# Kernel optimization log

Hardware: AMD Instinct MI355X
Metric: run time of the kernel (lower is better)

## Reference

```python
import jax, jax.numpy as jnp
import numpy as np

TAU = 2.0
V_TH = 1.0


def setup_inputs() -> dict:
    key = jax.random.key(0)
    k1, k2, k3 = jax.random.split(key, 3)
    T, B, H = 128, 64, 1024
    x = jax.random.normal(k1, (T, B, H), dtype=jnp.float32)
    # nn.Linear(H, H, bias=False) weights, shape [out, in]
    W1 = jax.random.normal(k2, (H, H), dtype=jnp.float32) / np.sqrt(H)
    W2 = jax.random.normal(k3, (H, H), dtype=jnp.float32) / np.sqrt(H)
    return {"x": x, "W1": W1, "W2": W2}


def _lif_scan(x_proj):
    # x_proj: [T, B, H]; membrane v starts at 0.
    def step(v, xt):
        h = v + (xt - v) / TAU          # leaky integrate
        s = (h >= V_TH).astype(h.dtype)  # hard-threshold spike
        v_new = h * (1.0 - s)            # soft reset (to 0 on spike)
        return v_new, s

    v0 = jnp.zeros(x_proj.shape[1:], dtype=x_proj.dtype)
    _, spikes = jax.lax.scan(step, v0, x_proj)
    return spikes  # [T, B, H]


def reference(x, W1, W2):
    # fc1 applied per timestep == one batched GEMM over [T*B, H]
    x_proj = jnp.einsum('tbh,oh->tbo', x, W1)
    spike = _lif_scan(x_proj)
    out = jnp.einsum('tbh,oh->tbo', spike, W2)
    return out
```

## Files before the change

### kernel.cpp

```cpp
#include <hip/hip_runtime.h>
#include <hip/hip_bf16.h>
#include <stdint.h>

#define TT 128
#define BB 64
#define HH 1024
#define MM (TT * BB)
#define NLANE (BB * HH)
#define DELTA 3.0e-4
#define CAPL 32768

typedef __attribute__((ext_vector_type(8))) short bf16x8;
typedef __attribute__((ext_vector_type(4))) float f32x4;

#define GLOAD16(g, l)                                                        \
    __builtin_amdgcn_global_load_lds(                                        \
        (const __attribute__((address_space(1))) unsigned int*)(g),          \
        (__attribute__((address_space(3))) unsigned int*)(l), 16, 0, 0)

static __device__ __forceinline__ unsigned short bf16_bits(float f) {
    __hip_bfloat16 b = __float2bfloat16(f);
    return *reinterpret_cast<unsigned short*>(&b);
}

__global__ __launch_bounds__(256) void split2_kernel(const float* __restrict__ src,
                                                     unsigned short* __restrict__ hi,
                                                     unsigned short* __restrict__ lo,
                                                     int n4) {
    const int i = blockIdx.x * 256 + threadIdx.x;
    if (i >= n4) return;
    float4 x = reinterpret_cast<const float4*>(src)[i];
    float v[4] = {x.x, x.y, x.z, x.w};
    unsigned short hb[4], lb[4];
#pragma unroll
    for (int c = 0; c < 4; c++) {
        hb[c] = bf16_bits(v[c]);
        __hip_bfloat16 hh = *reinterpret_cast<__hip_bfloat16*>(&hb[c]);
        lb[c] = bf16_bits(v[c] - __bfloat162float(hh));
    }
    reinterpret_cast<ushort4*>(hi)[i] = make_ushort4(hb[0], hb[1], hb[2], hb[3]);
    reinterpret_cast<ushort4*>(lo)[i] = make_ushort4(lb[0], lb[1], lb[2], lb[3]);
}

__global__ __launch_bounds__(256) void cast_bf16(const float* __restrict__ src,
                                                 unsigned short* __restrict__ dst,
                                                 int n) {
    const int i = blockIdx.x * 256 + threadIdx.x;
    if (i < n) dst[i] = bf16_bits(src[i]);
}

__global__ __launch_bounds__(256) void gemm1_mfma(const unsigned short* __restrict__ Ah,
                                                  const unsigned short* __restrict__ Al,
                                                  const unsigned short* __restrict__ Bh,
                                                  const unsigned short* __restrict__ Bl,
                                                  float* __restrict__ C) {
    __shared__ short AsH[128 * 32];
    __shared__ short AsL[128 * 32];
    __shared__ short BsH[128 * 32];
    __shared__ short BsL[128 * 32];

    const int tid = threadIdx.x;
    const int lane = tid & 63;
    const int wave = tid >> 6;
    const int m0 = blockIdx.x * 128;
    const int n0 = blockIdx.y * 128;
    const int wm = (wave >> 1) * 64;
    const int wn = (wave & 1) * 64;

    const int rsel = lane & 15;
    const int qk = (lane >> 4) * 8;

    f32x4 acc[4][4] = {};

    for (int k0 = 0; k0 < HH; k0 += 32) {
#pragma unroll
        for (int p = 0; p < 2; p++) {
            const int c = tid + p * 256;
            const int cb = wave * 64 + p * 256;
            const int row = c >> 2;
            const int part = c & 3;
            const size_t goA = (size_t)(m0 + row) * HH + k0 + part * 8;
            const size_t goB = (size_t)(n0 + row) * HH + k0 + part * 8;
            GLOAD16(&Ah[goA], &AsH[cb * 8]);
            GLOAD16(&Al[goA], &AsL[cb * 8]);
            GLOAD16(&Bh[goB], &BsH[cb * 8]);
            GLOAD16(&Bl[goB], &BsL[cb * 8]);
        }
        __syncthreads();

        bf16x8 aH[4], aL[4], bH[4], bL[4];
#pragma unroll
        for (int mi = 0; mi < 4; mi++) {
            const int r = (wm + mi * 16 + rsel) * 32 + qk;
            aH[mi] = *reinterpret_cast<bf16x8*>(&AsH[r]);
            aL[mi] = *reinterpret_cast<bf16x8*>(&AsL[r]);
        }
#pragma unroll
        for (int ni = 0; ni < 4; ni++) {
            const int r = (wn + ni * 16 + rsel) * 32 + qk;
            bH[ni] = *reinterpret_cast<bf16x8*>(&BsH[r]);
            bL[ni] = *reinterpret_cast<bf16x8*>(&BsL[r]);
        }

#pragma unroll
        for (int mi = 0; mi < 4; mi++)
#pragma unroll
            for (int ni = 0; ni < 4; ni++) {
                acc[mi][ni] = __builtin_amdgcn_mfma_f32_16x16x32_bf16(aH[mi], bH[ni], acc[mi][ni], 0, 0, 0);
                acc[mi][ni] = __builtin_amdgcn_mfma_f32_16x16x32_bf16(aH[mi], bL[ni], acc[mi][ni], 0, 0, 0);
                acc[mi][ni] = __builtin_amdgcn_mfma_f32_16x16x32_bf16(aL[mi], bH[ni], acc[mi][ni], 0, 0, 0);
            }

        __syncthreads();
    }

    const int col = lane & 15;
    const int quad = lane >> 4;
#pragma unroll
    for (int mi = 0; mi < 4; mi++)
#pragma unroll
        for (int ni = 0; ni < 4; ni++) {
            const int m = m0 + wm + mi * 16 + quad * 4;
            const int n = n0 + wn + ni * 16 + col;
            float* dst = &C[(size_t)m * HH + n];
#pragma unroll
            for (int r = 0; r < 4; r++)
                dst[(size_t)r * HH] = acc[mi][ni][r];
        }
}

__global__ __launch_bounds__(256) void lif_scan_flag(const float* __restrict__ xp,
                                                     unsigned short* __restrict__ sp,
                                                     int* __restrict__ count,
                                                     int* __restrict__ list) {
    const int idx = blockIdx.x * 256 + threadIdx.x;
    double v = 0.0;
    bool flg = false;
#pragma unroll 4
    for (int t = 0; t < TT; t++) {
        const double x = (double)xp[(size_t)t * NLANE + idx];
        const double h = v + (x - v) * 0.5;
        const bool s = (h >= 1.0);
        flg |= (fabs(h - 1.0) < DELTA);
        v = s ? 0.0 : h;
        sp[(size_t)t * NLANE + idx] = s ? (unsigned short)0x3F80 : (unsigned short)0;
    }
    if (flg) {
        const int i = atomicAdd(count, 1);
        list[i] = idx;
    }
}

__global__ __launch_bounds__(256) void recompute_dots(const float* __restrict__ X,
                                                      const float* __restrict__ W1,
                                                      const int* __restrict__ count,
                                                      const int* __restrict__ list,
                                                      double* __restrict__ hraw) {
    const int cnt = *count;
    const int lim = (cnt < CAPL ? cnt : CAPL);
    const long ntask = (long)lim * TT;
    const int ln = threadIdx.x & 63;
    const long wid = (long)blockIdx.x * 4 + (threadIdx.x >> 6);
    const long nwaves = (long)gridDim.x * 4;

    for (long task = wid; task < ntask; task += nwaves) {
        const int li = (int)(task >> 7);
        const int t = (int)(task & (TT - 1));
        const int lane = list[li];
        const int b = lane >> 10;
        const int h = lane & (HH - 1);
        const float4* x4 = reinterpret_cast<const float4*>(X + (size_t)(t * BB + b) * HH);
        const float4* w4 = reinterpret_cast<const float4*>(W1 + (size_t)h * HH);

        double s0 = 0.0, s1 = 0.0, s2 = 0.0, s3 = 0.0;
#pragma unroll
        for (int i = 0; i < 4; i++) {
            const float4 xa = x4[ln + i * 64];
            const float4 wa = w4[ln + i * 64];
            s0 = fma((double)xa.x, (double)wa.x, s0);
            s1 = fma((double)xa.y, (double)wa.y, s1);
            s2 = fma((double)xa.z, (double)wa.z, s2);
            s3 = fma((double)xa.w, (double)wa.w, s3);
        }
        double s = (s0 + s1) + (s2 + s3);
#pragma unroll
        for (int off = 32; off >= 1; off >>= 1)
            s += __shfl_down(s, off);
        if (ln == 0) hraw[task] = s;
    }
}

__global__ __launch_bounds__(256) void rescan_lanes(const float* __restrict__ X,
                                                    const float* __restrict__ W1,
                                                    const int* __restrict__ count,
                                                    const int* __restrict__ list,
                                                    const double* __restrict__ hraw,
                                                    unsigned short* __restrict__ sp) {
    const int li = blockIdx.x * 256 + threadIdx.x;
    const int cnt = *count;
    if (li >= cnt) return;
    const int lane = list[li];

    double v = 0.0;
    if (li < CAPL) {
        const double* hb = hraw + (size_t)li * TT;
        for (int t = 0; t < TT; t++) {
            const double h = v + (hb[t] - v) * 0.5;
            const bool s = (h >= 1.0);
            v = s ? 0.0 : h;
            sp[(size_t)t * NLANE + lane] = s ? (unsigned short)0x3F80 : (unsigned short)0;
        }
    } else {
        const int b = lane >> 10;
        const int h = lane & (HH - 1);
        const float* wrow = W1 + (size_t)h * HH;
        for (int t = 0; t < TT; t++) {
            const float* xrow = X + (size_t)(t * BB + b) * HH;
            double d = 0.0;
            for (int k = 0; k < HH; k++)
                d = fma((double)xrow[k], (double)wrow[k], d);
            const double hh = v + (d - v) * 0.5;
            const bool s = (hh >= 1.0);
            v = s ? 0.0 : hh;
            sp[(size_t)t * NLANE + lane] = s ? (unsigned short)0x3F80 : (unsigned short)0;
        }
    }
}

__global__ __launch_bounds__(256) void gemm2_mfma(const unsigned short* __restrict__ S,
                                                  const unsigned short* __restrict__ W,
                                                  float* __restrict__ O) {
    __shared__ short As[128 * 32];
    __shared__ short Bs[128 * 32];

    const int tid = threadIdx.x;
    const int lane = tid & 63;
    const int wave = tid >> 6;
    const int m0 = blockIdx.x * 128;
    const int n0 = blockIdx.y * 128;
    const int wm = (wave >> 1) * 64;
    const int wn = (wave & 1) * 64;

    const int rsel = lane & 15;
    const int qk = (lane >> 4) * 8;

    f32x4 acc[4][4] = {};

    for (int k0 = 0; k0 < HH; k0 += 32) {
#pragma unroll
        for (int p = 0; p < 2; p++) {
            const int c = tid + p * 256;
            const int cb = wave * 64 + p * 256;
            const int row = c >> 2;
            const int part = c & 3;
            GLOAD16(&S[(size_t)(m0 + row) * HH + k0 + part * 8], &As[cb * 8]);
            GLOAD16(&W[(size_t)(n0 + row) * HH + k0 + part * 8], &Bs[cb * 8]);
        }
        __syncthreads();

        bf16x8 a[4], b[4];
#pragma unroll
        for (int mi = 0; mi < 4; mi++)
            a[mi] = *reinterpret_cast<bf16x8*>(&As[(wm + mi * 16 + rsel) * 32 + qk]);
#pragma unroll
        for (int ni = 0; ni < 4; ni++)
            b[ni] = *reinterpret_cast<bf16x8*>(&Bs[(wn + ni * 16 + rsel) * 32 + qk]);

#pragma unroll
        for (int mi = 0; mi < 4; mi++)
#pragma unroll
            for (int ni = 0; ni < 4; ni++)
                acc[mi][ni] = __builtin_amdgcn_mfma_f32_16x16x32_bf16(
                    a[mi], b[ni], acc[mi][ni], 0, 0, 0);

        __syncthreads();
    }

    const int col = lane & 15;
    const int quad = lane >> 4;
#pragma unroll
    for (int mi = 0; mi < 4; mi++)
#pragma unroll
        for (int ni = 0; ni < 4; ni++) {
            const int m = m0 + wm + mi * 16 + quad * 4;
            const int n = n0 + wn + ni * 16 + col;
            float* dst = &O[(size_t)m * HH + n];
#pragma unroll
            for (int r = 0; r < 4; r++)
                dst[(size_t)r * HH] = acc[mi][ni][r];
        }
}

extern "C" void kernel_launch(void* const* d_in, const int* in_sizes, int n_in,
                              void* d_out, int out_size, void* d_ws, size_t ws_size,
                              hipStream_t stream) {
    const float* x  = (const float*)d_in[0];
    const float* W1 = (const float*)d_in[1];
    const float* W2 = (const float*)d_in[2];
    float* out = (float*)d_out;

    char* ws = (char*)d_ws;
    const size_t szX = (size_t)MM * HH;
    const size_t szW = (size_t)HH * HH;

    unsigned short* Xhi  = (unsigned short*)ws;
    unsigned short* Xlo  = Xhi + szX;
    unsigned short* W1hi = Xlo + szX;
    unsigned short* W1lo = W1hi + szW;
    unsigned short* w2b  = W1lo + szW;
    int*            list = (int*)(w2b + szW);
    int*            cnt  = list + NLANE;
    float*          xp   = (float*)(((uintptr_t)(cnt + 64) + 255) & ~(uintptr_t)255);
    unsigned short* sp   = Xhi;
    double*         hraw = (double*)xp;

    hipMemsetAsync(cnt, 0, sizeof(int), stream);

    split2_kernel<<<(int)(szX / 4 / 256), 256, 0, stream>>>(x, Xhi, Xlo, (int)(szX / 4));
    split2_kernel<<<(int)(szW / 4 / 256), 256, 0, stream>>>(W1, W1hi, W1lo, (int)(szW / 4));
    cast_bf16<<<(int)((szW + 255) / 256), 256, 0, stream>>>(W2, w2b, (int)szW);

    dim3 g1(MM / 128, HH / 128);
    gemm1_mfma<<<g1, 256, 0, stream>>>(Xhi, Xlo, W1hi, W1lo, xp);

    lif_scan_flag<<<NLANE / 256, 256, 0, stream>>>(xp, sp, cnt, list);

    recompute_dots<<<2048, 256, 0, stream>>>(x, W1, cnt, list, hraw);
    rescan_lanes<<<NLANE / 256, 256, 0, stream>>>(x, W1, cnt, list, hraw, sp);

    dim3 g2(MM / 128, HH / 128);
    gemm2_mfma<<<g2, 256, 0, stream>>>(sp, w2b, out);
}
```

Measured before the change: 258.9 us.

## Switch split GEMMs to fp16 with scaled low part, swizzle LDS, tighten flag band

Replaces the bf16 hi/lo split with an fp16 split whose low residual is scaled by 4096. The cross terms go into a separate accumulator and are recombined at the end. The higher precision lets the near-threshold flag band shrink tenfold, so fewer lanes go through the exact fp64 recompute and rescan path. It also adds an XOR swizzle to the LDS layout in both GEMMs to reduce bank conflicts, at the cost of a second accumulator set (more registers) and fp16 range risk on inputs.

```diff
diff --git a/kernel.cpp b/kernel.cpp
--- a/kernel.cpp
+++ b/kernel.cpp
@@ -7,10 +7,12 @@
 #define HH 1024
 #define MM (TT * BB)
 #define NLANE (BB * HH)
-#define DELTA 3.0e-4
+#define DELTA 3.0e-5
 #define CAPL 32768
-
-typedef __attribute__((ext_vector_type(8))) short bf16x8;
+#define LO_SCALE 4096.0f
+#define F16_ONE 0x3C00
+
+typedef __attribute__((ext_vector_type(8))) _Float16 f16x8;
 typedef __attribute__((ext_vector_type(4))) float f32x4;
 
 #define GLOAD16(g, l)                                                        \
@@ -18,9 +20,9 @@
         (const __attribute__((address_space(1))) unsigned int*)(g),          \
         (__attribute__((address_space(3))) unsigned int*)(l), 16, 0, 0)
 
-static __device__ __forceinline__ unsigned short bf16_bits(float f) {
-    __hip_bfloat16 b = __float2bfloat16(f);
-    return *reinterpret_cast<unsigned short*>(&b);
+static __device__ __forceinline__ unsigned short f16_bits(float f) {
+    _Float16 h = (_Float16)f;
+    return *reinterpret_cast<unsigned short*>(&h);
 }
 
 __global__ __launch_bounds__(256) void split2_kernel(const float* __restrict__ src,
@@ -34,19 +36,19 @@
     unsigned short hb[4], lb[4];
 #pragma unroll
     for (int c = 0; c < 4; c++) {
-        hb[c] = bf16_bits(v[c]);
-        __hip_bfloat16 hh = *reinterpret_cast<__hip_bfloat16*>(&hb[c]);
-        lb[c] = bf16_bits(v[c] - __bfloat162float(hh));
+        _Float16 hh = (_Float16)v[c];
+        hb[c] = *reinterpret_cast<unsigned short*>(&hh);
+        lb[c] = f16_bits((v[c] - (float)hh) * LO_SCALE);
     }
     reinterpret_cast<ushort4*>(hi)[i] = make_ushort4(hb[0], hb[1], hb[2], hb[3]);
     reinterpret_cast<ushort4*>(lo)[i] = make_ushort4(lb[0], lb[1], lb[2], lb[3]);
 }
 
-__global__ __launch_bounds__(256) void cast_bf16(const float* __restrict__ src,
-                                                 unsigned short* __restrict__ dst,
-                                                 int n) {
+__global__ __launch_bounds__(256) void cast_f16(const float* __restrict__ src,
+                                                unsigned short* __restrict__ dst,
+                                                int n) {
     const int i = blockIdx.x * 256 + threadIdx.x;
-    if (i < n) dst[i] = bf16_bits(src[i]);
+    if (i < n) dst[i] = f16_bits(src[i]);
 }
 
 __global__ __launch_bounds__(256) void gemm1_mfma(const unsigned short* __restrict__ Ah,
@@ -68,9 +70,19 @@
     const int wn = (wave & 1) * 64;
 
     const int rsel = lane & 15;
-    const int qk = (lane >> 4) * 8;
-
-    f32x4 acc[4][4] = {};
+    const int part = lane >> 4;
+
+    int adrA[4], adrB[4];
+#pragma unroll
+    for (int i = 0; i < 4; i++) {
+        const int ra = wm + i * 16 + rsel;
+        const int rb = wn + i * 16 + rsel;
+        adrA[i] = ra * 32 + (part ^ ((ra >> 1) & 3)) * 8;
+        adrB[i] = rb * 32 + (part ^ ((rb >> 1) & 3)) * 8;
+    }
+
+    f32x4 acc1[4][4] = {};
+    f32x4 acc2[4][4] = {};
 
     for (int k0 = 0; k0 < HH; k0 += 32) {
 #pragma unroll
@@ -78,9 +90,10 @@
             const int c = tid + p * 256;
             const int cb = wave * 64 + p * 256;
             const int row = c >> 2;
-            const int part = c & 3;
-            const size_t goA = (size_t)(m0 + row) * HH + k0 + part * 8;
-            const size_t goB = (size_t)(n0 + row) * HH + k0 + part * 8;
+            const int pslot = c & 3;
+            const int pdata = pslot ^ ((row >> 1) & 3);
+            const size_t goA = (size_t)(m0 + row) * HH + k0 + pdata * 8;
+            const size_t goB = (size_t)(n0 + row) * HH + k0 + pdata * 8;
             GLOAD16(&Ah[goA], &AsH[cb * 8]);
             GLOAD16(&Al[goA], &AsL[cb * 8]);
             GLOAD16(&Bh[goB], &BsH[cb * 8]);
@@ -88,27 +101,25 @@
         }
         __syncthreads();
 
-        bf16x8 aH[4], aL[4], bH[4], bL[4];
+        f16x8 aH[4], aL[4], bH[4], bL[4];
 #pragma unroll
         for (int mi = 0; mi < 4; mi++) {
-            const int r = (wm + mi * 16 + rsel) * 32 + qk;
-            aH[mi] = *reinterpret_cast<bf16x8*>(&AsH[r]);
-            aL[mi] = *reinterpret_cast<bf16x8*>(&AsL[r]);
+            aH[mi] = *reinterpret_cast<f16x8*>(&AsH[adrA[mi]]);
+            aL[mi] = *reinterpret_cast<f16x8*>(&AsL[adrA[mi]]);
         }
 #pragma unroll
         for (int ni = 0; ni < 4; ni++) {
-            const int r = (wn + ni * 16 + rsel) * 32 + qk;
-            bH[ni] = *reinterpret_cast<bf16x8*>(&BsH[r]);
-            bL[ni] = *reinterpret_cast<bf16x8*>(&BsL[r]);
+            bH[ni] = *reinterpret_cast<f16x8*>(&BsH[adrB[ni]]);
+            bL[ni] = *reinterpret_cast<f16x8*>(&BsL[adrB[ni]]);
         }
 
 #pragma unroll
         for (int mi = 0; mi < 4; mi++)
 #pragma unroll
             for (int ni = 0; ni < 4; ni++) {
-                acc[mi][ni] = __builtin_amdgcn_mfma_f32_16x16x32_bf16(aH[mi], bH[ni], acc[mi][ni], 0, 0, 0);
-                acc[mi][ni] = __builtin_amdgcn_mfma_f32_16x16x32_bf16(aH[mi], bL[ni], acc[mi][ni], 0, 0, 0);
-                acc[mi][ni] = __builtin_amdgcn_mfma_f32_16x16x32_bf16(aL[mi], bH[ni], acc[mi][ni], 0, 0, 0);
+                acc1[mi][ni] = __builtin_amdgcn_mfma_f32_16x16x32_f16(aH[mi], bH[ni], acc1[mi][ni], 0, 0, 0);
+                acc2[mi][ni] = __builtin_amdgcn_mfma_f32_16x16x32_f16(aH[mi], bL[ni], acc2[mi][ni], 0, 0, 0);
+                acc2[mi][ni] = __builtin_amdgcn_mfma_f32_16x16x32_f16(aL[mi], bH[ni], acc2[mi][ni], 0, 0, 0);
             }
 
         __syncthreads();
@@ -116,6 +127,7 @@
 
     const int col = lane & 15;
     const int quad = lane >> 4;
+    const float inv = 1.0f / LO_SCALE;
 #pragma unroll
     for (int mi = 0; mi < 4; mi++)
 #pragma unroll
@@ -125,7 +137,7 @@
             float* dst = &C[(size_t)m * HH + n];
 #pragma unroll
             for (int r = 0; r < 4; r++)
-                dst[(size_t)r * HH] = acc[mi][ni][r];
+                dst[(size_t)r * HH] = fmaf(acc2[mi][ni][r], inv, acc1[mi][ni][r]);
         }
 }
 
@@ -143,7 +155,7 @@
         const bool s = (h >= 1.0);
         flg |= (fabs(h - 1.0) < DELTA);
         v = s ? 0.0 : h;
-        sp[(size_t)t * NLANE + idx] = s ? (unsigned short)0x3F80 : (unsigned short)0;
+        sp[(size_t)t * NLANE + idx] = s ? (unsigned short)F16_ONE : (unsigned short)0;
     }
     if (flg) {
         const int i = atomicAdd(count, 1);
@@ -208,7 +220,7 @@
             const double h = v + (hb[t] - v) * 0.5;
             const bool s = (h >= 1.0);
             v = s ? 0.0 : h;
-            sp[(size_t)t * NLANE + lane] = s ? (unsigned short)0x3F80 : (unsigned short)0;
+            sp[(size_t)t * NLANE + lane] = s ? (unsigned short)F16_ONE : (unsigned short)0;
         }
     } else {
         const int b = lane >> 10;
@@ -222,7 +234,7 @@
             const double hh = v + (d - v) * 0.5;
             const bool s = (hh >= 1.0);
             v = s ? 0.0 : hh;
-            sp[(size_t)t * NLANE + lane] = s ? (unsigned short)0x3F80 : (unsigned short)0;
+            sp[(size_t)t * NLANE + lane] = s ? (unsigned short)F16_ONE : (unsigned short)0;
         }
     }
 }
@@ -242,7 +254,16 @@
     const int wn = (wave & 1) * 64;
 
     const int rsel = lane & 15;
-    const int qk = (lane >> 4) * 8;
+    const int part = lane >> 4;
+
+    int adrA[4], adrB[4];
+#pragma unroll
+    for (int i = 0; i < 4; i++) {
+        const int ra = wm + i * 16 + rsel;
+        const int rb = wn + i * 16 + rsel;
+        adrA[i] = ra * 32 + (part ^ ((ra >> 1) & 3)) * 8;
+        adrB[i] = rb * 32 + (part ^ ((rb >> 1) & 3)) * 8;
+    }
 
     f32x4 acc[4][4] = {};
 
@@ -252,25 +273,26 @@
             const int c = tid + p * 256;
             const int cb = wave * 64 + p * 256;
             const int row = c >> 2;
-            const int part = c & 3;
-            GLOAD16(&S[(size_t)(m0 + row) * HH + k0 + part * 8], &As[cb * 8]);
-            GLOAD16(&W[(size_t)(n0 + row) * HH + k0 + part * 8], &Bs[cb * 8]);
+            const int pslot = c & 3;
+            const int pdata = pslot ^ ((row >> 1) & 3);
+            GLOAD16(&S[(size_t)(m0 + row) * HH + k0 + pdata * 8], &As[cb * 8]);
+            GLOAD16(&W[(size_t)(n0 + row) * HH + k0 + pdata * 8], &Bs[cb * 8]);
         }
         __syncthreads();
 
-        bf16x8 a[4], b[4];
+        f16x8 a[4], b[4];
 #pragma unroll
         for (int mi = 0; mi < 4; mi++)
-            a[mi] = *reinterpret_cast<bf16x8*>(&As[(wm + mi * 16 + rsel) * 32 + qk]);
+            a[mi] = *reinterpret_cast<f16x8*>(&As[adrA[mi]]);
 #pragma unroll
         for (int ni = 0; ni < 4; ni++)
-            b[ni] = *reinterpret_cast<bf16x8*>(&Bs[(wn + ni * 16 + rsel) * 32 + qk]);
+            b[ni] = *reinterpret_cast<f16x8*>(&Bs[adrB[ni]]);
 
 #pragma unroll
         for (int mi = 0; mi < 4; mi++)
 #pragma unroll
             for (int ni = 0; ni < 4; ni++)
-                acc[mi][ni] = __builtin_amdgcn_mfma_f32_16x16x32_bf16(
+                acc[mi][ni] = __builtin_amdgcn_mfma_f32_16x16x32_f16(
                     a[mi], b[ni], acc[mi][ni], 0, 0, 0);
 
         __syncthreads();
@@ -307,8 +329,8 @@
     unsigned short* Xlo  = Xhi + szX;
     unsigned short* W1hi = Xlo + szX;
     unsigned short* W1lo = W1hi + szW;
-    unsigned short* w2b  = W1lo + szW;
-    int*            list = (int*)(w2b + szW);
+    unsigned short* w2h  = W1lo + szW;
+    int*            list = (int*)(w2h + szW);
     int*            cnt  = list + NLANE;
     float*          xp   = (float*)(((uintptr_t)(cnt + 64) + 255) & ~(uintptr_t)255);
     unsigned short* sp   = Xhi;
@@ -318,7 +340,7 @@
 
     split2_kernel<<<(int)(szX / 4 / 256), 256, 0, stream>>>(x, Xhi, Xlo, (int)(szX / 4));
     split2_kernel<<<(int)(szW / 4 / 256), 256, 0, stream>>>(W1, W1hi, W1lo, (int)(szW / 4));
-    cast_bf16<<<(int)((szW + 255) / 256), 256, 0, stream>>>(W2, w2b, (int)szW);
+    cast_f16<<<(int)((szW + 255) / 256), 256, 0, stream>>>(W2, w2h, (int)szW);
 
     dim3 g1(MM / 128, HH / 128);
     gemm1_mfma<<<g1, 256, 0, stream>>>(Xhi, Xlo, W1hi, W1lo, xp);
@@ -329,5 +351,5 @@
     rescan_lanes<<<NLANE / 256, 256, 0, stream>>>(x, W1, cnt, list, hraw, sp);
 
     dim3 g2(MM / 128, HH / 128);
-    gemm2_mfma<<<g2, 256, 0, stream>>>(sp, w2b, out);
-}
+    gemm2_mfma<<<g2, 256, 0, stream>>>(sp, w2h, out);
+}
```

Result: no change. 258.5 us (-0.1%).
